# Performance work log

Measured on AMD Instinct MI355X. Metric: run time of the kernel, lower is better.

The kernel has to match this reference:

```python
import jax, jax.numpy as jnp
import numpy as np

B, T, DM, H = 2, 2048, 2048, 16
D = DM // H  # 128
STD = 0.02


def setup_inputs() -> dict:
    key = jax.random.key(0)
    ks = jax.random.split(key, 8)
    inner = H * D
    x = jax.random.normal(ks[0], (B, T, DM), jnp.float32)
    state = jnp.zeros((B, H, D, D), jnp.float32)
    Wq = jax.random.normal(ks[1], (inner, DM), jnp.float32) * STD
    Wk = jax.random.normal(ks[2], (inner, DM), jnp.float32) * STD
    Wv = jax.random.normal(ks[3], (inner, DM), jnp.float32) * STD
    Wa = jax.random.normal(ks[4], (inner, DM), jnp.float32) * STD
    ba = jnp.zeros((inner,), jnp.float32)
    Wb = jax.random.normal(ks[5], (H, DM), jnp.float32) * STD
    bb = jnp.zeros((H,), jnp.float32)
    Wg = jax.random.normal(ks[6], (inner, DM), jnp.float32) * STD
    bg = jnp.zeros((inner,), jnp.float32)
    Wo = jax.random.normal(ks[7], (DM, inner), jnp.float32) * STD
    return {"x": x, "state": state, "Wq": Wq, "Wk": Wk, "Wv": Wv,
            "Wa": Wa, "ba": ba, "Wb": Wb, "bb": bb, "Wg": Wg, "bg": bg, "Wo": Wo}


def _l2norm(t):
    # matches torch F.normalize(p=2, dim=-1, eps=1e-12)
    n = jnp.sqrt(jnp.sum(t * t, axis=-1, keepdims=True))
    return t / jnp.maximum(n, 1e-12)


def reference(x, state, Wq, Wk, Wv, Wa, ba, Wb, bb, Wg, bg, Wo):
    b, t, _ = x.shape
    q = _l2norm((x @ Wq.T).reshape(b, t, H, D))
    k = _l2norm((x @ Wk.T).reshape(b, t, H, D))
    v = (x @ Wv.T).reshape(b, t, H, D)
    alpha = jax.nn.sigmoid(x @ Wa.T + ba).reshape(b, t, H, D)
    beta = jax.nn.sigmoid(x @ Wb.T + bb)  # (B,T,H)

    def step(S, inp):
        q_t, k_t, v_t, a_t, b_t = inp  # (B,H,D) x4, (B,H)
        Sk = jnp.einsum('bhij,bhj->bhi', S, k_t)
        delta = v_t - Sk
        S = a_t[..., None] * S + (b_t[..., None] * delta)[..., None] * k_t[:, :, None, :]
        out_t = jnp.einsum('bhij,bhj->bhi', S, q_t)
        return S, out_t

    xs = tuple(jnp.moveaxis(a, 1, 0) for a in (q, k, v, alpha, beta))
    _, outs = jax.lax.scan(step, state, xs)  # outs: (T,B,H,D)
    out = jnp.moveaxis(outs, 0, 1)  # (B,T,H,D)
    g = jax.nn.sigmoid(x @ Wg.T + bg).reshape(b, t, H, D)
    out = (out * g).reshape(b, t, H * D) @ Wo.T
    return out
```

## Files before the change

### kernel.cpp

```cpp
#include <hip/hip_runtime.h>
#include <hip/hip_bf16.h>

typedef short short8 __attribute__((ext_vector_type(8)));
typedef float f32x4 __attribute__((ext_vector_type(4)));

#define DEV __device__ __forceinline__
#define AS1 __attribute__((address_space(1)))
#define AS3 __attribute__((address_space(3)))

DEV void async_load16(const void* g, void* l) {
    __builtin_amdgcn_global_load_lds((const AS1 unsigned int*)g, (AS3 unsigned int*)l, 16, 0, 0);
}

template <int CTRL>
DEV float dpp_add16(float v) {
    int t = __builtin_amdgcn_update_dpp(0, __float_as_int(v), CTRL, 0xf, 0xf, true);
    return v + __int_as_float(t);
}
DEV float row_sum16(float v) {
    v = dpp_add16<0x128>(v);
    v = dpp_add16<0x124>(v);
    v = dpp_add16<0x122>(v);
    v = dpp_add16<0x121>(v);
    return v;
}

__global__ __launch_bounds__(256) void cast_bf16_kernel(const float* __restrict__ in,
                                                        __hip_bfloat16* __restrict__ out, int n) {
    int i = (blockIdx.x * 256 + threadIdx.x) * 4;
    if (i < n) {
        float4 v = *(const float4*)&in[i];
        out[i + 0] = __float2bfloat16(v.x);
        out[i + 1] = __float2bfloat16(v.y);
        out[i + 2] = __float2bfloat16(v.z);
        out[i + 3] = __float2bfloat16(v.w);
    }
}

template <int EPI>
__global__ __launch_bounds__(256) void gemm_nt(const short* __restrict__ A,
                                               const short* __restrict__ Bm,
                                               float* __restrict__ C,
                                               const float* __restrict__ bias,
                                               int M, int N, int K) {
    __shared__ short lda[128 * 32];
    __shared__ short ldb[128 * 32];
    const int tid  = threadIdx.x;
    const int lane = tid & 63;
    const int wave = tid >> 6;

    const int nbx = M >> 7;
    const int wg  = blockIdx.y * gridDim.x + blockIdx.x;
    const int nwg = gridDim.x * gridDim.y;
    const int cpx = nwg >> 3;
    const int swz = (wg & 7) * cpx + (wg >> 3);
    const int m0 = (swz & (nbx - 1)) * 128;
    const int n0 = (swz / nbx) * 128;

    const int wm = (wave >> 1) * 64;
    const int wn = (wave & 1) * 64;
    f32x4 acc[4][4] = {};

    const int sr = tid >> 2;
    const int sc = (tid & 3) * 8;
    const short* Ab  = A  + (size_t)(m0 + sr) * K + sc;
    const short* Ab2 = Ab + (size_t)64 * K;
    const short* Bb  = Bm + (size_t)(n0 + sr) * K + sc;
    const short* Bb2 = Bb + (size_t)64 * K;
    short* la  = &lda[tid * 8];
    short* la2 = &lda[(tid + 256) * 8];
    short* lb  = &ldb[tid * 8];
    short* lb2 = &ldb[(tid + 256) * 8];

    const int fk = (lane >> 4) * 8;
    const int fr = lane & 15;

    for (int k0 = 0; k0 < K; k0 += 32) {
        async_load16(Ab + k0,  la);
        async_load16(Ab2 + k0, la2);
        async_load16(Bb + k0,  lb);
        async_load16(Bb2 + k0, lb2);
        __syncthreads();
        short8 af[4], bfr[4];
#pragma unroll
        for (int i = 0; i < 4; i++) af[i]  = *(const short8*)&lda[(wm + i * 16 + fr) * 32 + fk];
#pragma unroll
        for (int j = 0; j < 4; j++) bfr[j] = *(const short8*)&ldb[(wn + j * 16 + fr) * 32 + fk];
#pragma unroll
        for (int i = 0; i < 4; i++)
#pragma unroll
            for (int j = 0; j < 4; j++)
                acc[i][j] = __builtin_amdgcn_mfma_f32_16x16x32_bf16(af[i], bfr[j], acc[i][j], 0, 0, 0);
        __syncthreads();
    }

    const int er = (lane >> 4) * 4;
    const int ec = lane & 15;
#pragma unroll
    for (int i = 0; i < 4; i++) {
        const int gr = m0 + wm + i * 16 + er;
#pragma unroll
        for (int j = 0; j < 4; j++) {
            const int gc = n0 + wn + j * 16 + ec;
            float bia = 0.f;
            if constexpr (EPI == 1) bia = bias[gc];
#pragma unroll
            for (int r = 0; r < 4; r++) {
                float v = acc[i][j][r];
                if constexpr (EPI == 1) v = 1.f / (1.f + __expf(-(v + bia)));
                C[(size_t)(gr + r) * N + gc] = v;
            }
        }
    }
}

__global__ __launch_bounds__(256) void l2norm_kernel(float* __restrict__ buf) {
    const int row  = blockIdx.x * 4 + (threadIdx.x >> 6);
    const int lane = threadIdx.x & 63;
    float* p = &buf[(size_t)row * 128 + lane * 2];
    float2 v = *(float2*)p;
    float s = v.x * v.x + v.y * v.y;
#pragma unroll
    for (int off = 1; off < 64; off <<= 1) s += __shfl_xor(s, off);
    const float inv = 1.f / fmaxf(sqrtf(s), 1e-12f);
    v.x *= inv; v.y *= inv;
    *(float2*)p = v;
}

__global__ __launch_bounds__(256) void beta_kernel(const float* __restrict__ x,
                                                   const float* __restrict__ Wb,
                                                   const float* __restrict__ bb,
                                                   float* __restrict__ beta) {
    __shared__ float xs[16 * 132];
    const int tid = threadIdx.x;
    const float* xr = &x[(size_t)blockIdx.x * 2048];
#pragma unroll
    for (int i = tid; i < 512; i += 256) {
        float4 v = ((const float4*)xr)[i];
        const int j = i * 4;
        *(float4*)&xs[(j >> 7) * 132 + (j & 127)] = v;
    }
    __syncthreads();
    const int n = tid >> 4, ks = tid & 15;
    const float* w  = &Wb[(size_t)n * 2048 + ks * 128];
    const float* xx = &xs[ks * 132];
    float s = 0.f;
#pragma unroll 8
    for (int j = 0; j < 128; j++) s += xx[j] * w[j];
    s += __shfl_xor(s, 1); s += __shfl_xor(s, 2);
    s += __shfl_xor(s, 4); s += __shfl_xor(s, 8);
    if (ks == 0) beta[(size_t)blockIdx.x * 16 + n] = 1.f / (1.f + __expf(-(s + bb[n])));
}

__global__ __launch_bounds__(256)
__attribute__((amdgpu_waves_per_eu(1, 1)))
void recurrence_kernel(
        const float* __restrict__ S0, const float* __restrict__ qn, const float* __restrict__ kn,
        const float* __restrict__ vv, const float* __restrict__ adec, const float* __restrict__ bet,
        const float* __restrict__ gg, __hip_bfloat16* __restrict__ o) {
    __shared__ __hip_bfloat16 lout[4][64][4];

    const int bh  = blockIdx.x & 31;
    const int rb8 = blockIdx.x >> 5;
    const int b = bh >> 4, h = bh & 15;
    const int lane = threadIdx.x & 63;
    const int wave = threadIdx.x >> 6;
    const int r = lane >> 4;
    const int c = lane & 15;
    const int i0 = rb8 * 16 + wave * 4;
    const int i = i0 + r;

    f32x4 S40, S41;
    {
        const float* s0 = &S0[((size_t)(bh * 128 + i)) * 128 + c * 8];
        S40 = *(const f32x4*)s0;
        S41 = *(const f32x4*)(s0 + 4);
    }

    const size_t hb = (size_t)(b * 2048) * 16 + h;
    const unsigned SB = 16 * 128 * 4;
    const float* kbase = kn   + hb * 128;
    const float* qbase = qn   + hb * 128;
    const float* vbase = vv   + hb * 128;
    const float* abase = adec + hb * 128;
    const float* gbase = gg   + hb * 128;
    const float* bbase = bet  + hb;
    char* ob = (char*)(o + hb * 128 + i0);

    unsigned voff_kq = (unsigned)(c * 32);
    unsigned voff_i  = (unsigned)(i * 4);
    unsigned voff_b  = 0;

    f32x4 kA0, kA1, qA0, qA1; float vA, aA, gA, bA;
    f32x4 kB0, kB1, qB0, qB1; float vB, aB, gB, bB;
    f32x4 kC0, kC1, qC0, qC1; float vC, aC, gC, bC;
    f32x4 kD0, kD1, qD0, qD1; float vD, aD, gD, bD;

#define ISSUE(SET)                                                              \
    asm volatile("global_load_dwordx4 %0, %2, %3\n\t"                           \
                 "global_load_dwordx4 %1, %2, %3 offset:16"                     \
                 : "=v"(k##SET##0), "=v"(k##SET##1)                             \
                 : "v"(voff_kq), "s"(kbase));                                   \
    asm volatile("global_load_dwordx4 %0, %2, %3\n\t"                           \
                 "global_load_dwordx4 %1, %2, %3 offset:16"                     \
                 : "=v"(q##SET##0), "=v"(q##SET##1)                             \
                 : "v"(voff_kq), "s"(qbase));                                   \
    asm volatile("global_load_dword %0, %1, %2"                                 \
                 : "=v"(v##SET) : "v"(voff_i), "s"(vbase));                     \
    asm volatile("global_load_dword %0, %1, %2"                                 \
                 : "=v"(a##SET) : "v"(voff_i), "s"(abase));                     \
    asm volatile("global_load_dword %0, %1, %2"                                 \
                 : "=v"(g##SET) : "v"(voff_i), "s"(gbase));                     \
    asm volatile("global_load_dword %0, %1, %2"                                 \
                 : "=v"(b##SET) : "v"(voff_b), "s"(bbase));

#define ADV() { voff_kq += SB; voff_i += SB; voff_b += 64; }

    ISSUE(A); ADV();
    ISSUE(B); ADV();
    ISSUE(C); ADV();
    ISSUE(D); ADV();

#define BODY(SLOT, SET)                                                   \
    {                                                                     \
        asm volatile("s_waitcnt vmcnt(24)" ::: "memory");                 \
        __builtin_amdgcn_sched_barrier(0);                                \
        f32x4 ps = S40 * k##SET##0;                                       \
        ps = S41 * k##SET##1 + ps;                                        \
        float p = row_sum16((ps[0] + ps[1]) + (ps[2] + ps[3]));           \
        const float coef = b##SET * (v##SET - p);                         \
        S40 = a##SET * S40 + coef * k##SET##0;                            \
        S41 = a##SET * S41 + coef * k##SET##1;                            \
        f32x4 os = S40 * q##SET##0;                                       \
        os = S41 * q##SET##1 + os;                                        \
        float ov = row_sum16((os[0] + os[1]) + (os[2] + os[3]));          \
        if (c == 0) lout[wave][(SLOT)][r] = __float2bfloat16(ov * g##SET);\
        ISSUE(SET);                                                       \
        ADV();                                                            \
    }

    for (int tb = 0; tb < 2048; tb += 64) {
        for (int tt = 0; tt < 64; tt += 4) {
            BODY(tt,     A);
            BODY(tt + 1, B);
            BODY(tt + 2, C);
            BODY(tt + 3, D);
        }
        uint2 pk = *(const uint2*)&lout[wave][lane][0];
        *(uint2*)(ob + (size_t)(tb + lane) * 4096) = pk;
    }
#undef BODY
#undef ADV
#undef ISSUE
}

extern "C" void kernel_launch(void* const* d_in, const int* in_sizes, int n_in,
                              void* d_out, int out_size, void* d_ws, size_t ws_size,
                              hipStream_t stream) {
    const float* x  = (const float*)d_in[0];
    const float* S0 = (const float*)d_in[1];
    const float* Wq = (const float*)d_in[2];
    const float* Wk = (const float*)d_in[3];
    const float* Wv = (const float*)d_in[4];
    const float* Wa = (const float*)d_in[5];
    const float* ba = (const float*)d_in[6];
    const float* Wb = (const float*)d_in[7];
    const float* bb = (const float*)d_in[8];
    const float* Wg = (const float*)d_in[9];
    const float* bg = (const float*)d_in[10];
    const float* Wo = (const float*)d_in[11];
    float* out = (float*)d_out;

    const int M = 4096, N = 2048, K = 2048;
    const size_t SLACK = 8 * 16 * 128 * 4;

    size_t off = 0;
    auto alloc = [&](size_t bytes) {
        void* p = (char*)d_ws + off;
        off += (bytes + 255) & ~(size_t)255;
        return p;
    };
    short* x_bf  = (short*)alloc((size_t)M * K * 2);
    short* Wq_bf = (short*)alloc((size_t)N * K * 2);
    short* Wk_bf = (short*)alloc((size_t)N * K * 2);
    short* Wv_bf = (short*)alloc((size_t)N * K * 2);
    short* Wa_bf = (short*)alloc((size_t)N * K * 2);
    short* Wg_bf = (short*)alloc((size_t)N * K * 2);
    short* Wo_bf = (short*)alloc((size_t)N * K * 2);
    float* qb    = (float*)alloc((size_t)M * N * 4 + SLACK);
    float* kb    = (float*)alloc((size_t)M * N * 4 + SLACK);
    float* vb    = (float*)alloc((size_t)M * N * 4 + SLACK);
    float* ab    = (float*)alloc((size_t)M * N * 4 + SLACK);
    float* gb    = (float*)alloc((size_t)M * N * 4 + SLACK);
    float* betab = (float*)alloc((size_t)M * 16 * 4 + 32768);

    cast_bf16_kernel<<<dim3((M * K / 4 + 255) / 256), dim3(256), 0, stream>>>(x,  (__hip_bfloat16*)x_bf,  M * K);
    cast_bf16_kernel<<<dim3((N * K / 4 + 255) / 256), dim3(256), 0, stream>>>(Wq, (__hip_bfloat16*)Wq_bf, N * K);
    cast_bf16_kernel<<<dim3((N * K / 4 + 255) / 256), dim3(256), 0, stream>>>(Wk, (__hip_bfloat16*)Wk_bf, N * K);
    cast_bf16_kernel<<<dim3((N * K / 4 + 255) / 256), dim3(256), 0, stream>>>(Wv, (__hip_bfloat16*)Wv_bf, N * K);
    cast_bf16_kernel<<<dim3((N * K / 4 + 255) / 256), dim3(256), 0, stream>>>(Wa, (__hip_bfloat16*)Wa_bf, N * K);
    cast_bf16_kernel<<<dim3((N * K / 4 + 255) / 256), dim3(256), 0, stream>>>(Wg, (__hip_bfloat16*)Wg_bf, N * K);
    cast_bf16_kernel<<<dim3((N * K / 4 + 255) / 256), dim3(256), 0, stream>>>(Wo, (__hip_bfloat16*)Wo_bf, N * K);

    dim3 gdim(M / 128, N / 128), bdim(256);
    gemm_nt<0><<<gdim, bdim, 0, stream>>>(x_bf, Wq_bf, qb, nullptr, M, N, K);
    gemm_nt<0><<<gdim, bdim, 0, stream>>>(x_bf, Wk_bf, kb, nullptr, M, N, K);
    gemm_nt<0><<<gdim, bdim, 0, stream>>>(x_bf, Wv_bf, vb, nullptr, M, N, K);
    gemm_nt<1><<<gdim, bdim, 0, stream>>>(x_bf, Wa_bf, ab, ba, M, N, K);
    gemm_nt<1><<<gdim, bdim, 0, stream>>>(x_bf, Wg_bf, gb, bg, M, N, K);

    l2norm_kernel<<<dim3(M * 16 / 4), dim3(256), 0, stream>>>(qb);
    l2norm_kernel<<<dim3(M * 16 / 4), dim3(256), 0, stream>>>(kb);
    beta_kernel<<<dim3(M), dim3(256), 0, stream>>>(x, Wb, bb, betab);

    __hip_bfloat16* o_bf = (__hip_bfloat16*)x_bf;
    recurrence_kernel<<<dim3(256), dim3(256), 0, stream>>>(S0, qb, kb, vb, ab, betab, gb, o_bf);

    gemm_nt<0><<<gdim, bdim, 0, stream>>>((const short*)o_bf, Wo_bf, out, nullptr, M, N, K);
}
```

Baseline: 793.2 us.

## Fuse five projection GEMMs into one wide GEMM with interleaved output layout

Concatenates Wq/Wk/Wv/Wa/Wg into one contiguous bf16 weight block and runs a single GEMM with N=10240. The sigmoid+bias epilogue is applied per column tile, and the output is stored as one interleaved row-major buffer that the l2norm and recurrence kernels index with a new stride. The six weight casts are merged into one launch and the two l2norm launches into one. This removes launch overhead and repeated x reads, but gives the recurrence a larger row stride and replaces the sched_barrier in its loop with register constraints.

```diff
diff --git a/kernel.cpp b/kernel.cpp
--- a/kernel.cpp
+++ b/kernel.cpp
@@ -37,11 +37,28 @@
     }
 }
 
+__global__ __launch_bounds__(256) void cast6_kernel(const float* __restrict__ s0, const float* __restrict__ s1,
+                                                    const float* __restrict__ s2, const float* __restrict__ s3,
+                                                    const float* __restrict__ s4, const float* __restrict__ s5,
+                                                    __hip_bfloat16* __restrict__ dst) {
+    const int sec = blockIdx.x >> 12;
+    const int loc = blockIdx.x & 4095;
+    const float* s = sec == 0 ? s0 : sec == 1 ? s1 : sec == 2 ? s2 : sec == 3 ? s3 : sec == 4 ? s4 : s5;
+    const int i = (loc * 256 + threadIdx.x) * 4;
+    float4 v = *(const float4*)&s[i];
+    __hip_bfloat16* o = dst + (size_t)sec * 4194304 + i;
+    o[0] = __float2bfloat16(v.x);
+    o[1] = __float2bfloat16(v.y);
+    o[2] = __float2bfloat16(v.z);
+    o[3] = __float2bfloat16(v.w);
+}
+
 template <int EPI>
 __global__ __launch_bounds__(256) void gemm_nt(const short* __restrict__ A,
                                                const short* __restrict__ Bm,
                                                float* __restrict__ C,
-                                               const float* __restrict__ bias,
+                                               const float* __restrict__ bias1,
+                                               const float* __restrict__ bias2,
                                                int M, int N, int K) {
     __shared__ short lda[128 * 32];
     __shared__ short ldb[128 * 32];
@@ -96,6 +113,12 @@
 
     const int er = (lane >> 4) * 4;
     const int ec = lane & 15;
+    bool sig = false;
+    const float* bp = nullptr;
+    if constexpr (EPI == 2) {
+        sig = (n0 >= 6144);
+        if (sig) bp = (n0 >= 8192) ? (bias2 + (n0 - 8192)) : (bias1 + (n0 - 6144));
+    }
 #pragma unroll
     for (int i = 0; i < 4; i++) {
         const int gr = m0 + wm + i * 16 + er;
@@ -103,11 +126,11 @@
         for (int j = 0; j < 4; j++) {
             const int gc = n0 + wn + j * 16 + ec;
             float bia = 0.f;
-            if constexpr (EPI == 1) bia = bias[gc];
+            if constexpr (EPI == 2) { if (sig) bia = bp[wn + j * 16 + ec]; }
 #pragma unroll
             for (int r = 0; r < 4; r++) {
                 float v = acc[i][j][r];
-                if constexpr (EPI == 1) v = 1.f / (1.f + __expf(-(v + bia)));
+                if constexpr (EPI == 2) { if (sig) v = 1.f / (1.f + __expf(-(v + bia))); }
                 C[(size_t)(gr + r) * N + gc] = v;
             }
         }
@@ -115,9 +138,10 @@
 }
 
 __global__ __launch_bounds__(256) void l2norm_kernel(float* __restrict__ buf) {
-    const int row  = blockIdx.x * 4 + (threadIdx.x >> 6);
+    const int id   = blockIdx.x * 4 + (threadIdx.x >> 6);
     const int lane = threadIdx.x & 63;
-    float* p = &buf[(size_t)row * 128 + lane * 2];
+    const int t = id >> 5, rem = id & 31;
+    float* p = &buf[(size_t)t * 10240 + (rem >> 4) * 2048 + (rem & 15) * 128 + lane * 2];
     float2 v = *(float2*)p;
     float s = v.x * v.x + v.y * v.y;
 #pragma unroll
@@ -155,9 +179,8 @@
 __global__ __launch_bounds__(256)
 __attribute__((amdgpu_waves_per_eu(1, 1)))
 void recurrence_kernel(
-        const float* __restrict__ S0, const float* __restrict__ qn, const float* __restrict__ kn,
-        const float* __restrict__ vv, const float* __restrict__ adec, const float* __restrict__ bet,
-        const float* __restrict__ gg, __hip_bfloat16* __restrict__ o) {
+        const float* __restrict__ S0, const float* __restrict__ qall,
+        const float* __restrict__ bet, __hip_bfloat16* __restrict__ o) {
     __shared__ __hip_bfloat16 lout[4][64][4];
 
     const int bh  = blockIdx.x & 31;
@@ -177,15 +200,15 @@
         S41 = *(const f32x4*)(s0 + 4);
     }
 
-    const size_t hb = (size_t)(b * 2048) * 16 + h;
-    const unsigned SB = 16 * 128 * 4;
-    const float* kbase = kn   + hb * 128;
-    const float* qbase = qn   + hb * 128;
-    const float* vbase = vv   + hb * 128;
-    const float* abase = adec + hb * 128;
-    const float* gbase = gg   + hb * 128;
-    const float* bbase = bet  + hb;
-    char* ob = (char*)(o + hb * 128 + i0);
+    const unsigned SB = 10240 * 4;
+    const float* rowb = qall + (size_t)(b * 2048) * 10240 + h * 128;
+    const float* qbase = rowb;
+    const float* kbase = rowb + 2048;
+    const float* vbase = rowb + 4096;
+    const float* abase = rowb + 6144;
+    const float* gbase = rowb + 8192;
+    const float* bbase = bet + (size_t)(b * 2048) * 16 + h;
+    char* ob = (char*)(o + ((size_t)(b * 2048) * 16 + h) * 128 + i0);
 
     unsigned voff_kq = (unsigned)(c * 32);
     unsigned voff_i  = (unsigned)(i * 4);
@@ -223,8 +246,11 @@
 
 #define BODY(SLOT, SET)                                                   \
     {                                                                     \
-        asm volatile("s_waitcnt vmcnt(24)" ::: "memory");                 \
-        __builtin_amdgcn_sched_barrier(0);                                \
+        asm volatile("s_waitcnt vmcnt(24)");                              \
+        asm volatile("" : "+v"(k##SET##0), "+v"(k##SET##1),               \
+                          "+v"(q##SET##0), "+v"(q##SET##1),               \
+                          "+v"(v##SET), "+v"(a##SET),                     \
+                          "+v"(g##SET), "+v"(b##SET));                    \
         f32x4 ps = S40 * k##SET##0;                                       \
         ps = S41 * k##SET##1 + ps;                                        \
         float p = row_sum16((ps[0] + ps[1]) + (ps[2] + ps[3]));           \
@@ -271,8 +297,9 @@
     const float* Wo = (const float*)d_in[11];
     float* out = (float*)d_out;
 
-    const int M = 4096, N = 2048, K = 2048;
-    const size_t SLACK = 8 * 16 * 128 * 4;
+    const int M = 4096, K = 2048;
+    const int NF = 10240;
+    const size_t SLACK = 8 * (size_t)NF * 4;
 
     size_t off = 0;
     auto alloc = [&](size_t bytes) {
@@ -281,40 +308,22 @@
         return p;
     };
     short* x_bf  = (short*)alloc((size_t)M * K * 2);
-    short* Wq_bf = (short*)alloc((size_t)N * K * 2);
-    short* Wk_bf = (short*)alloc((size_t)N * K * 2);
-    short* Wv_bf = (short*)alloc((size_t)N * K * 2);
-    short* Wa_bf = (short*)alloc((size_t)N * K * 2);
-    short* Wg_bf = (short*)alloc((size_t)N * K * 2);
-    short* Wo_bf = (short*)alloc((size_t)N * K * 2);
-    float* qb    = (float*)alloc((size_t)M * N * 4 + SLACK);
-    float* kb    = (float*)alloc((size_t)M * N * 4 + SLACK);
-    float* vb    = (float*)alloc((size_t)M * N * 4 + SLACK);
-    float* ab    = (float*)alloc((size_t)M * N * 4 + SLACK);
-    float* gb    = (float*)alloc((size_t)M * N * 4 + SLACK);
+    short* W_bf  = (short*)alloc((size_t)6 * K * K * 2);
+    float* qall  = (float*)alloc((size_t)M * NF * 4 + SLACK);
     float* betab = (float*)alloc((size_t)M * 16 * 4 + 32768);
 
-    cast_bf16_kernel<<<dim3((M * K / 4 + 255) / 256), dim3(256), 0, stream>>>(x,  (__hip_bfloat16*)x_bf,  M * K);
-    cast_bf16_kernel<<<dim3((N * K / 4 + 255) / 256), dim3(256), 0, stream>>>(Wq, (__hip_bfloat16*)Wq_bf, N * K);
-    cast_bf16_kernel<<<dim3((N * K / 4 + 255) / 256), dim3(256), 0, stream>>>(Wk, (__hip_bfloat16*)Wk_bf, N * K);
-    cast_bf16_kernel<<<dim3((N * K / 4 + 255) / 256), dim3(256), 0, stream>>>(Wv, (__hip_bfloat16*)Wv_bf, N * K);
-    cast_bf16_kernel<<<dim3((N * K / 4 + 255) / 256), dim3(256), 0, stream>>>(Wa, (__hip_bfloat16*)Wa_bf, N * K);
-    cast_bf16_kernel<<<dim3((N * K / 4 + 255) / 256), dim3(256), 0, stream>>>(Wg, (__hip_bfloat16*)Wg_bf, N * K);
-    cast_bf16_kernel<<<dim3((N * K / 4 + 255) / 256), dim3(256), 0, stream>>>(Wo, (__hip_bfloat16*)Wo_bf, N * K);
-
-    dim3 gdim(M / 128, N / 128), bdim(256);
-    gemm_nt<0><<<gdim, bdim, 0, stream>>>(x_bf, Wq_bf, qb, nullptr, M, N, K);
-    gemm_nt<0><<<gdim, bdim, 0, stream>>>(x_bf, Wk_bf, kb, nullptr, M, N, K);
-    gemm_nt<0><<<gdim, bdim, 0, stream>>>(x_bf, Wv_bf, vb, nullptr, M, N, K);
-    gemm_nt<1><<<gdim, bdim, 0, stream>>>(x_bf, Wa_bf, ab, ba, M, N, K);
-    gemm_nt<1><<<gdim, bdim, 0, stream>>>(x_bf, Wg_bf, gb, bg, M, N, K);
-
-    l2norm_kernel<<<dim3(M * 16 / 4), dim3(256), 0, stream>>>(qb);
-    l2norm_kernel<<<dim3(M * 16 / 4), dim3(256), 0, stream>>>(kb);
+    cast_bf16_kernel<<<dim3(M * K / 1024), dim3(256), 0, stream>>>(x, (__hip_bfloat16*)x_bf, M * K);
+    cast6_kernel<<<dim3(6 * 4096), dim3(256), 0, stream>>>(Wq, Wk, Wv, Wa, Wg, Wo, (__hip_bfloat16*)W_bf);
+
+    gemm_nt<2><<<dim3(M / 128, NF / 128), dim3(256), 0, stream>>>(
+        x_bf, W_bf, qall, ba, bg, M, NF, K);
+
+    l2norm_kernel<<<dim3(32768), dim3(256), 0, stream>>>(qall);
     beta_kernel<<<dim3(M), dim3(256), 0, stream>>>(x, Wb, bb, betab);
 
     __hip_bfloat16* o_bf = (__hip_bfloat16*)x_bf;
-    recurrence_kernel<<<dim3(256), dim3(256), 0, stream>>>(S0, qb, kb, vb, ab, betab, gb, o_bf);
-
-    gemm_nt<0><<<gdim, bdim, 0, stream>>>((const short*)o_bf, Wo_bf, out, nullptr, M, N, K);
-}
+    recurrence_kernel<<<dim3(256), dim3(256), 0, stream>>>(S0, qall, betab, o_bf);
+
+    gemm_nt<0><<<dim3(M / 128, K / 128), dim3(256), 0, stream>>>(
+        (const short*)o_bf, W_bf + (size_t)5 * K * K, out, nullptr, nullptr, M, K, K);
+}
```

Result: faster. 749.7 us (-5.5%).
